# Kernel tuning notes

Measured on AMD Instinct MI355X. Metric: run time of the kernel, lower is better.

The kernel has to match this reference:

```python
import jax, jax.numpy as jnp
import numpy as np

B, S, DIM = 2, 2048, 2048
H, KVH, HD = 16, 4, 128
WIN = 512
ROPE_BASE = 10000.0
EPS = 1.1920928955078125e-07  # torch F.rms_norm default eps for fp32


def setup_inputs() -> dict:
    key = jax.random.key(0)
    ks = jax.random.split(key, 6)
    kv_dim = KVH * HD
    sc = lambda fan_in: 1.0 / np.sqrt(fan_in)
    return {
        "x": jax.random.normal(ks[0], (B, S, DIM), jnp.float32),
        "Wq": jax.random.normal(ks[1], (DIM, DIM), jnp.float32) * sc(DIM),
        "Wk": jax.random.normal(ks[2], (kv_dim, DIM), jnp.float32) * sc(DIM),
        "Wv": jax.random.normal(ks[3], (kv_dim, DIM), jnp.float32) * sc(DIM),
        "Wo": jax.random.normal(ks[4], (DIM, DIM), jnp.float32) * sc(DIM),
        "q_gain": jnp.ones((H,), jnp.float32),
    }


def _rms_norm(x):
    return x * jax.lax.rsqrt(jnp.mean(x * x, axis=-1, keepdims=True) + EPS)


def _rope_tables(seqlen, dtype):
    half = HD // 2
    inv_freq = ROPE_BASE ** (-jnp.arange(0, half, dtype=jnp.float32) / half)
    freqs = jnp.arange(seqlen, dtype=jnp.float32)[:, None] * inv_freq[None, :]  # [S, HD/2]
    return jnp.cos(freqs).astype(dtype), jnp.sin(freqs).astype(dtype)


def _apply_rotary(x, cos, sin):
    # x: [B, H, S, HD]; cos/sin: [S, HD/2]
    half = x.shape[-1] // 2
    x1, x2 = x[..., :half], x[..., half:]
    c = cos[None, None, :, :]
    s = sin[None, None, :, :]
    return jnp.concatenate([x1 * c + x2 * s, -x1 * s + x2 * c], axis=-1)


def reference(x, Wq, Wk, Wv, Wo, q_gain):
    bsz, seqlen, dim = x.shape
    q = jnp.einsum("bsd,ed->bse", x, Wq).reshape(bsz, seqlen, H, HD).transpose(0, 2, 1, 3)
    k = jnp.einsum("bsd,ed->bse", x, Wk).reshape(bsz, seqlen, KVH, HD).transpose(0, 2, 1, 3)
    v = jnp.einsum("bsd,ed->bse", x, Wv).reshape(bsz, seqlen, KVH, HD).transpose(0, 2, 1, 3)

    q = _rms_norm(q)
    k = _rms_norm(k)

    cos, sin = _rope_tables(seqlen, q.dtype)
    q = _apply_rotary(q, cos, sin)
    k = _apply_rotary(k, cos, sin)

    q = q * q_gain[None, :, None, None]

    # GQA: expand kv heads to match query heads
    rep = H // KVH
    k = jnp.repeat(k, rep, axis=1)
    v = jnp.repeat(v, rep, axis=1)

    row = jnp.arange(seqlen)[:, None]
    col = jnp.arange(seqlen)[None, :]
    mask = (col <= row) & (col >= row - WIN + 1)  # [S, S]

    scale = 1.0 / np.sqrt(HD)
    scores = jnp.einsum("bhsd,bhtd->bhst", q, k) * scale
    scores = jnp.where(mask[None, None, :, :], scores, -jnp.inf)
    attn = jax.nn.softmax(scores, axis=-1)
    y = jnp.einsum("bhst,bhtd->bhsd", attn, v)  # [B, H, S, HD]

    y = y.transpose(0, 2, 1, 3).reshape(bsz, seqlen, dim)
    return jnp.einsum("bsd,ed->bse", y, Wo)
```

## Files before the change

### kernel.cpp

```cpp
#include <hip/hip_runtime.h>

#define S_LEN 2048
#define DIM   2048
#define NH    16
#define NKV   4
#define HD    128
#define WIN   512
#define BATCH 2

typedef __bf16 bf16x8 __attribute__((ext_vector_type(8)));
typedef __bf16 bf16x4 __attribute__((ext_vector_type(4)));
typedef float  f32x4  __attribute__((ext_vector_type(4)));

union U8 { bf16x8 v; bf16x4 h[2]; };

__device__ inline void async_load16(const void* g, void* l) {
  __builtin_amdgcn_global_load_lds(
      (const __attribute__((address_space(1))) unsigned int*)g,
      (__attribute__((address_space(3))) unsigned int*)l, 16, 0, 0);
}

__global__ __launch_bounds__(256) void preprocess_kernel(
    const float* __restrict__ x,
    const float* __restrict__ Wq, const float* __restrict__ Wk,
    const float* __restrict__ Wv, const float* __restrict__ Wo,
    __bf16* __restrict__ xb, __bf16* __restrict__ wqkv, __bf16* __restrict__ wob,
    float* __restrict__ cosT, float* __restrict__ sinT) {
  const int blk = blockIdx.x, tid = threadIdx.x;
  if (blk < 8192) {
    int i = blk * 256 + tid;
    float4 v = ((const float4*)x)[i];
    bf16x4 o;
    o[0] = (__bf16)v.x; o[1] = (__bf16)v.y; o[2] = (__bf16)v.z; o[3] = (__bf16)v.w;
    ((bf16x4*)xb)[i] = o;
  } else if (blk < 18432) {
    int i = (blk - 8192) * 256 + tid;
    int orow = i >> 9, c = i & 511;
    const float* src;
    __bf16* dst;
    long soff;
    if (orow < 2048) {
      int n = orow & 127;
      int sr = (orow & ~127) + ((n >> 5) << 4) + (n & 15) + (((n >> 4) & 1) << 6);
      src = Wq; soff = (long)sr * 512 + c; dst = wqkv + (long)orow * 2048;
    } else if (orow < 2560) {
      int lr = orow - 2048, n = lr & 127;
      int sr = (lr & ~127) + ((n >> 5) << 4) + (n & 15) + (((n >> 4) & 1) << 6);
      src = Wk; soff = (long)sr * 512 + c; dst = wqkv + (long)orow * 2048;
    } else if (orow < 3072) {
      src = Wv; soff = (long)(orow - 2560) * 512 + c; dst = wqkv + (long)orow * 2048;
    } else {
      src = Wo; soff = (long)(orow - 3072) * 512 + c; dst = wob + (long)(orow - 3072) * 2048;
    }
    float4 v = ((const float4*)src)[soff];
    bf16x4 o;
    o[0] = (__bf16)v.x; o[1] = (__bf16)v.y; o[2] = (__bf16)v.z; o[3] = (__bf16)v.w;
    ((bf16x4*)dst)[c] = o;
  } else {
    int idx = (blk - 18432) * 256 + tid;
    int s = idx >> 6, d = idx & 63;
    float f = (float)s * powf(10000.f, -(float)d * (1.f / 64.f));
    float sn, cs;
    sincosf(f, &sn, &cs);
    cosT[idx] = cs;
    sinT[idx] = sn;
  }
}

__global__ __launch_bounds__(256) void gemm_bt(
    const __bf16* __restrict__ A, const __bf16* __restrict__ Bt,
    float* __restrict__ C, int M, int N, int K) {
  __shared__ __bf16 As[128 * 32];
  __shared__ __bf16 Bs[128 * 32];
  const int t = threadIdx.x;
  const int wid = t >> 6, lane = t & 63;
  const int quad = lane >> 4, l15 = lane & 15;
  const long m0 = (long)blockIdx.x * 128, n0 = (long)blockIdx.y * 128;
  const int wm = (wid >> 1) * 64, wn = (wid & 1) * 64;

  const __bf16* ga = A + (m0 + (t >> 2)) * (long)K + (t & 3) * 8;
  const __bf16* gb = Bt + (n0 + (t >> 2)) * (long)K + (t & 3) * 8;
  char* lA = (char*)As + wid * 1024;
  char* lB = (char*)Bs + wid * 1024;
  const long rstride = 64L * K;

  f32x4 zero = {0.f, 0.f, 0.f, 0.f};
  f32x4 acc[4][4];
#pragma unroll
  for (int i = 0; i < 4; ++i)
#pragma unroll
    for (int j = 0; j < 4; ++j) acc[i][j] = zero;

  for (int k0 = 0; k0 < K; k0 += 32) {
    async_load16(ga + k0, lA);
    async_load16(ga + k0 + rstride, lA + 4096);
    async_load16(gb + k0, lB);
    async_load16(gb + k0 + rstride, lB + 4096);
    __syncthreads();
    bf16x8 af[4], bfr[4];
#pragma unroll
    for (int i = 0; i < 4; ++i) {
      af[i] = *(const bf16x8*)(As + (wm + i * 16 + l15) * 32 + quad * 8);
      bfr[i] = *(const bf16x8*)(Bs + (wn + i * 16 + l15) * 32 + quad * 8);
    }
#pragma unroll
    for (int i = 0; i < 4; ++i)
#pragma unroll
      for (int j = 0; j < 4; ++j)
        acc[i][j] = __builtin_amdgcn_mfma_f32_16x16x32_bf16(af[i], bfr[j], acc[i][j], 0, 0, 0);
    __syncthreads();
  }

#pragma unroll
  for (int i = 0; i < 4; ++i)
#pragma unroll
    for (int j = 0; j < 4; ++j)
#pragma unroll
      for (int r = 0; r < 4; ++r)
        C[(m0 + wm + i * 16 + quad * 4 + r) * (long)N + n0 + wn + j * 16 + l15] = acc[i][j][r];
}

__global__ __launch_bounds__(256) void gemm_qkv(
    const __bf16* __restrict__ A, const __bf16* __restrict__ Bt,
    const float* __restrict__ gain,
    const float* __restrict__ cosT, const float* __restrict__ sinT,
    __bf16* __restrict__ Qo, __bf16* __restrict__ Ko, __bf16* __restrict__ Vt) {
  __shared__ __bf16 As[128 * 32];
  __shared__ __bf16 Bs[128 * 32];
  const int K = 2048;
  const int t = threadIdx.x;
  const int wid = t >> 6, lane = t & 63;
  const int quad = lane >> 4, l15 = lane & 15;
  const long m0 = (long)blockIdx.x * 128, n0 = (long)blockIdx.y * 128;
  const int wm = (wid >> 1) * 64, wn = (wid & 1) * 64;

  const __bf16* ga = A + (m0 + (t >> 2)) * (long)K + (t & 3) * 8;
  const __bf16* gb = Bt + (n0 + (t >> 2)) * (long)K + (t & 3) * 8;
  char* lA = (char*)As + wid * 1024;
  char* lB = (char*)Bs + wid * 1024;
  const long rstride = 64L * K;

  f32x4 zero = {0.f, 0.f, 0.f, 0.f};
  f32x4 acc[4][4];
#pragma unroll
  for (int i = 0; i < 4; ++i)
#pragma unroll
    for (int j = 0; j < 4; ++j) acc[i][j] = zero;

  for (int k0 = 0; k0 < K; k0 += 32) {
    async_load16(ga + k0, lA);
    async_load16(ga + k0 + rstride, lA + 4096);
    async_load16(gb + k0, lB);
    async_load16(gb + k0 + rstride, lB + 4096);
    __syncthreads();
    bf16x8 af[4], bfr[4];
#pragma unroll
    for (int i = 0; i < 4; ++i) {
      af[i] = *(const bf16x8*)(As + (wm + i * 16 + l15) * 32 + quad * 8);
      bfr[i] = *(const bf16x8*)(Bs + (wn + i * 16 + l15) * 32 + quad * 8);
    }
#pragma unroll
    for (int i = 0; i < 4; ++i)
#pragma unroll
      for (int j = 0; j < 4; ++j)
        acc[i][j] = __builtin_amdgcn_mfma_f32_16x16x32_bf16(af[i], bfr[j], acc[i][j], 0, 0, 0);
    __syncthreads();
  }

  const int by = blockIdx.y;
  const int srow0 = (int)(m0 & 2047);
  const int bb = (int)(m0 >> 11);

  if (by >= 20) {
    const int kvh = by - 20;
    __bf16* Vb = Vt + ((long)(bb * NKV + kvh)) * HD * S_LEN;
#pragma unroll
    for (int i = 0; i < 4; ++i)
#pragma unroll
      for (int j = 0; j < 4; ++j) {
        int d = wn + j * 16 + l15;
        int s0 = srow0 + wm + i * 16 + quad * 4;
        bf16x4 o;
#pragma unroll
        for (int r = 0; r < 4; ++r) o[r] = (__bf16)acc[i][j][r];
        *(bf16x4*)(Vb + (long)d * S_LEN + s0) = o;
      }
  } else {
    float* sums = (float*)As;
#pragma unroll
    for (int i = 0; i < 4; ++i)
#pragma unroll
      for (int r = 0; r < 4; ++r) {
        float t2 = acc[i][0][r] * acc[i][0][r] + acc[i][1][r] * acc[i][1][r] +
                   acc[i][2][r] * acc[i][2][r] + acc[i][3][r] * acc[i][3][r];
#pragma unroll
        for (int off = 1; off < 16; off <<= 1) t2 += __shfl_xor(t2, off, 64);
        if (l15 == 0) sums[(wm + i * 16 + quad * 4 + r) * 2 + (wn >> 6)] = t2;
      }
    __syncthreads();

    float g;
    __bf16* base;
    if (by < 16) {
      g = gain[by] * 0.08838834764831845f;
      base = Qo + ((long)(bb * NH + by)) * S_LEN * HD;
    } else {
      g = 1.f;
      base = Ko + ((long)(bb * NKV + (by - 16))) * S_LEN * HD;
    }
#pragma unroll
    for (int i = 0; i < 4; ++i)
#pragma unroll
      for (int r = 0; r < 4; ++r) {
        int lrow = wm + i * 16 + quad * 4 + r;
        int srow = srow0 + lrow;
        float rs = rsqrtf((sums[lrow * 2] + sums[lrow * 2 + 1]) * (1.f / 128.f) +
                          1.1920928955078125e-07f);
#pragma unroll
        for (int a = 0; a < 2; ++a) {
          int dlow = (wn >> 1) + a * 16 + l15;
          float cv = cosT[srow * 64 + dlow];
          float sv = sinT[srow * 64 + dlow];
          float x1 = acc[i][2 * a][r] * rs;
          float x2 = acc[i][2 * a + 1][r] * rs;
          base[(long)srow * HD + wn + (2 * a) * 16 + l15] = (__bf16)((x1 * cv + x2 * sv) * g);
          base[(long)srow * HD + wn + (2 * a + 1) * 16 + l15] = (__bf16)((-x1 * sv + x2 * cv) * g);
        }
      }
  }
}

__global__ __launch_bounds__(256, 4) void attn_kernel(
    const __bf16* __restrict__ Q,
    const __bf16* __restrict__ K,
    const __bf16* __restrict__ Vt,
    const float* __restrict__ gain,
    __bf16* __restrict__ Y) {
  __shared__ __bf16 Ks[64 * 128];
  __shared__ __bf16 Vs[128 * 64];
  __shared__ __bf16 Ps[4][16 * 64];

  const int t = threadIdx.x;
  const int wid = t >> 6, lane = t & 63;
  const int quad = lane >> 4, l15 = lane & 15;
  const int qt_blk = 31 - blockIdx.x;
  const int h = blockIdx.y, b = blockIdx.z;
  const int kv = h >> 2;
  const int t0 = qt_blk * 64;
  const int r0 = t0 + wid * 16;

  const __bf16* Qb = Q + ((long)(b * NH + h)) * S_LEN * HD;
  const __bf16* Kb = K + ((long)(b * NKV + kv)) * S_LEN * HD;
  const __bf16* Vb = Vt + ((long)(b * NKV + kv)) * HD * S_LEN;
  const float M = 11.3137085f * fabsf(gain[h]);

  bf16x8 qf[4];
#pragma unroll
  for (int c = 0; c < 4; ++c)
    qf[c] = *(const bf16x8*)(Qb + (long)(r0 + l15) * HD + c * 32 + quad * 8);

  f32x4 zero = {0.f, 0.f, 0.f, 0.f};
  f32x4 acc[8];
#pragma unroll
  for (int d = 0; d < 8; ++d) acc[d] = zero;
  float lac = 0.f;

  int ksrc[4], vsrc[4];
#pragma unroll
  for (int j = 0; j < 4; ++j) {
    int kr = j * 16 + (t >> 4);
    ksrc[j] = kr * HD + (((t & 15) ^ (kr & 15)) << 3);
    int vd = j * 32 + (t >> 3);
    vsrc[j] = vd * S_LEN + (((t & 7) ^ (vd & 7)) << 3);
  }

  const int kstart = (t0 >= WIN) ? (t0 - WIN) : 0;
  const int ntiles = (t0 + 64 - kstart) >> 6;

  for (int it = 0; it < ntiles; ++it) {
    const int kt = kstart + it * 64;
#pragma unroll
    for (int j = 0; j < 4; ++j) {
      async_load16(Kb + (long)kt * HD + ksrc[j], (char*)Ks + j * 4096 + t * 16);
      async_load16(Vb + kt + vsrc[j], (char*)Vs + j * 4096 + t * 16);
    }
    __syncthreads();

    if (kt <= r0 + 15 && kt + 63 >= r0 - (WIN - 1)) {
#pragma unroll
      for (int kti = 0; kti < 4; ++kti) {
        bf16x8 kf[4];
#pragma unroll
        for (int c = 0; c < 4; ++c)
          kf[c] = *(const bf16x8*)(Ks + (kti * 16 + l15) * 128 +
                                   ((((c << 2) + quad) ^ l15) << 3));
        f32x4 sc = zero;
#pragma unroll
        for (int c = 0; c < 4; ++c)
          sc = __builtin_amdgcn_mfma_f32_16x16x32_bf16(kf[c], qf[c], sc, 0, 0, 0);
        const int qg = r0 + l15;
        const int kbase = kt + kti * 16 + quad * 4;
        bf16x4 pv;
#pragma unroll
        for (int r = 0; r < 4; ++r) {
          int key = kbase + r;
          float p = (key <= qg && key >= qg - (WIN - 1)) ? __expf(sc[r] - M) : 0.f;
          lac += p;
          pv[r] = (__bf16)p;
        }
        const int cb = kti * 4 + quad;
        *(bf16x4*)(&Ps[wid][l15 * 64 + ((cb ^ l15) << 2)]) = pv;
      }
      bf16x8 pf[2];
#pragma unroll
      for (int kc = 0; kc < 2; ++kc) {
        U8 u;
        u.h[0] = *(const bf16x4*)(&Ps[wid][l15 * 64 + (((kc * 8 + quad * 2) ^ l15) << 2)]);
        u.h[1] = *(const bf16x4*)(&Ps[wid][l15 * 64 + (((kc * 8 + quad * 2 + 1) ^ l15) << 2)]);
        pf[kc] = u.v;
      }
#pragma unroll
      for (int dt = 0; dt < 8; ++dt)
#pragma unroll
        for (int kc = 0; kc < 2; ++kc) {
          bf16x8 vf = *(const bf16x8*)(Vs + (dt * 16 + l15) * 64 +
                                       ((((kc << 2) + quad) ^ (l15 & 7)) << 3));
          acc[dt] = __builtin_amdgcn_mfma_f32_16x16x32_bf16(pf[kc], vf, acc[dt], 0, 0, 0);
        }
    }
    __syncthreads();
  }

  float s = lac;
  s += __shfl_xor(s, 16, 64);
  s += __shfl_xor(s, 32, 64);
  __bf16* Yb = Y + ((long)b * S_LEN) * DIM + h * HD;
#pragma unroll
  for (int r = 0; r < 4; ++r) {
    const int row = quad * 4 + r;
    float il = 1.f / __shfl(s, row, 64);
#pragma unroll
    for (int dt = 0; dt < 8; ++dt)
      Yb[(long)(r0 + row) * DIM + dt * 16 + l15] = (__bf16)(acc[dt][r] * il);
  }
}

extern "C" void kernel_launch(void* const* d_in, const int* in_sizes, int n_in,
                              void* d_out, int out_size, void* d_ws, size_t ws_size,
                              hipStream_t stream) {
  (void)in_sizes; (void)n_in; (void)out_size; (void)ws_size;
  const float* x  = (const float*)d_in[0];
  const float* Wq = (const float*)d_in[1];
  const float* Wk = (const float*)d_in[2];
  const float* Wv = (const float*)d_in[3];
  const float* Wo = (const float*)d_in[4];
  const float* qg = (const float*)d_in[5];
  float* out = (float*)d_out;

  char* ws = (char*)d_ws;
  size_t off = 0;
  auto alloc = [&](size_t bytes) -> void* {
    void* p = ws + off;
    off += (bytes + 255) & ~(size_t)255;
    return p;
  };
  __bf16* xb   = (__bf16*)alloc(8388608ull * 2);
  __bf16* wqkv = (__bf16*)alloc(3072ull * 2048 * 2);
  __bf16* wob  = (__bf16*)alloc(2048ull * 2048 * 2);
  __bf16* qo   = (__bf16*)alloc((size_t)BATCH * NH * S_LEN * HD * 2);
  __bf16* ko   = (__bf16*)alloc((size_t)BATCH * NKV * S_LEN * HD * 2);
  __bf16* vt   = (__bf16*)alloc((size_t)BATCH * NKV * HD * S_LEN * 2);
  float*  cosT = (float*)alloc(2048ull * 64 * 4);
  float*  sinT = (float*)alloc(2048ull * 64 * 4);
  __bf16* yb   = xb;

  preprocess_kernel<<<18944, 256, 0, stream>>>(x, Wq, Wk, Wv, Wo, xb, wqkv, wob,
                                               cosT, sinT);
  gemm_qkv<<<dim3(32, 24), 256, 0, stream>>>(xb, wqkv, qg, cosT, sinT, qo, ko, vt);
  attn_kernel<<<dim3(32, 16, 2), 256, 0, stream>>>(qo, ko, vt, qg, yb);
  gemm_bt<<<dim3(32, 16), 256, 0, stream>>>(yb, wob, out, 4096, 2048, 2048);
}
```

Before: 264.1 us.

## Rewrite QKV GEMM as 256x256 tile, double-buffered, swizzled LDS pipeline

The QKV projection GEMM moves from 128x128 tiles with 256 threads and a single LDS buffer to 256x256 tiles with 512 threads (8 waves). It uses 128 KB of dynamic shared memory for double-buffered K=64 stages, XOR-swizzled LDS columns, and interleaved MFMA and prefetch phases with s_setprio. This is meant to hide global-load latency, cut LDS bank conflicts and raise data reuse per tile. The epilogue is remapped so each block covers two heads. The grid drops to 192 blocks, which may underfill the CUs and raises register pressure from 128 accumulators per thread.

Measured after the change: 274.0 us. 3.7% more time.

```diff
diff --git a/kernel.cpp b/kernel.cpp
--- a/kernel.cpp
+++ b/kernel.cpp
@@ -120,111 +120,210 @@
         C[(m0 + wm + i * 16 + quad * 4 + r) * (long)N + n0 + wn + j * 16 + l15] = acc[i][j][r];
 }
 
-__global__ __launch_bounds__(256) void gemm_qkv(
+__global__ __launch_bounds__(512, 2) void gemm_qkv(
     const __bf16* __restrict__ A, const __bf16* __restrict__ Bt,
     const float* __restrict__ gain,
     const float* __restrict__ cosT, const float* __restrict__ sinT,
     __bf16* __restrict__ Qo, __bf16* __restrict__ Ko, __bf16* __restrict__ Vt) {
-  __shared__ __bf16 As[128 * 32];
-  __shared__ __bf16 Bs[128 * 32];
-  const int K = 2048;
+  extern __shared__ char smem[];
+  constexpr int K = 2048;
+  constexpr int NT = 32;
   const int t = threadIdx.x;
   const int wid = t >> 6, lane = t & 63;
   const int quad = lane >> 4, l15 = lane & 15;
-  const long m0 = (long)blockIdx.x * 128, n0 = (long)blockIdx.y * 128;
-  const int wm = (wid >> 1) * 64, wn = (wid & 1) * 64;
-
-  const __bf16* ga = A + (m0 + (t >> 2)) * (long)K + (t & 3) * 8;
-  const __bf16* gb = Bt + (n0 + (t >> 2)) * (long)K + (t & 3) * 8;
-  char* lA = (char*)As + wid * 1024;
-  char* lB = (char*)Bs + wid * 1024;
-  const long rstride = 64L * K;
+  const int wr = wid >> 2, wc = wid & 3;
+  const long m0 = (long)blockIdx.x * 256;
+  const long n0 = (long)blockIdx.y * 256;
+
+  const int srw = (wid << 3) + (lane >> 3);
+  const int c8 = (lane & 7) ^ ((lane >> 3) & 7);
+  const __bf16* ag = A + (m0 + srw) * (long)K + c8 * 8;
+  const __bf16* bg = Bt + (n0 + srw) * (long)K + c8 * 8;
+  char* const lbase = smem + (wid << 10);
+
+  auto stage = [&](int buf, int op, int h, int j, int kt) {
+    const __bf16* g = (op ? bg : ag) + (long)((h << 7) + (j << 6)) * K + (long)kt * 64;
+    async_load16(g, lbase + buf * 65536 + op * 32768 + h * 16384 + j * 8192);
+  };
+
+  const int swz = (l15 & 7) << 4;
+  const int col0 = (quad * 16) ^ swz;
+  const int col1 = (64 + quad * 16) ^ swz;
+  const char* const aBase = smem + wr * 16384;
+  const char* const bBase = smem + 32768 + (wc >> 1) * 16384;
+  const int brow = (wc & 1) << 6;
 
   f32x4 zero = {0.f, 0.f, 0.f, 0.f};
-  f32x4 acc[4][4];
-#pragma unroll
-  for (int i = 0; i < 4; ++i)
+  f32x4 acc[8][4];
+#pragma unroll
+  for (int i = 0; i < 8; ++i)
 #pragma unroll
     for (int j = 0; j < 4; ++j) acc[i][j] = zero;
 
-  for (int k0 = 0; k0 < K; k0 += 32) {
-    async_load16(ga + k0, lA);
-    async_load16(ga + k0 + rstride, lA + 4096);
-    async_load16(gb + k0, lB);
-    async_load16(gb + k0 + rstride, lB + 4096);
-    __syncthreads();
-    bf16x8 af[4], bfr[4];
+#pragma unroll
+  for (int b = 0; b < 2; ++b)
+#pragma unroll
+    for (int op = 0; op < 2; ++op)
+#pragma unroll
+      for (int h = 0; h < 2; ++h)
+#pragma unroll
+        for (int j = 0; j < 2; ++j) stage(b, op, h, j, b);
+  asm volatile("s_waitcnt vmcnt(8)" ::: "memory");
+  __builtin_amdgcn_s_barrier();
+
+  auto group = [&](const int buf, const int tt) {
+    const char* As = aBase + buf * 65536;
+    const char* Bs = bBase + buf * 65536;
+    const bool st = (tt + 2) < NT;
+    bf16x8 afl[4][2], afh[4][2], bfl[2][2], bfh[2][2];
 #pragma unroll
     for (int i = 0; i < 4; ++i) {
-      af[i] = *(const bf16x8*)(As + (wm + i * 16 + l15) * 32 + quad * 8);
-      bfr[i] = *(const bf16x8*)(Bs + (wn + i * 16 + l15) * 32 + quad * 8);
-    }
-#pragma unroll
-    for (int i = 0; i < 4; ++i)
-#pragma unroll
-      for (int j = 0; j < 4; ++j)
-        acc[i][j] = __builtin_amdgcn_mfma_f32_16x16x32_bf16(af[i], bfr[j], acc[i][j], 0, 0, 0);
-    __syncthreads();
+      afl[i][0] = *(const bf16x8*)(As + (i * 16 + l15) * 128 + col0);
+      afl[i][1] = *(const bf16x8*)(As + (i * 16 + l15) * 128 + col1);
+    }
+#pragma unroll
+    for (int j = 0; j < 2; ++j) {
+      bfl[j][0] = *(const bf16x8*)(Bs + (brow + j * 16 + l15) * 128 + col0);
+      bfl[j][1] = *(const bf16x8*)(Bs + (brow + j * 16 + l15) * 128 + col1);
+    }
+    __builtin_amdgcn_s_barrier();
+    asm volatile("s_waitcnt lgkmcnt(0)" ::: "memory");
+    __builtin_amdgcn_s_setprio(1);
+#pragma unroll
+    for (int kk = 0; kk < 2; ++kk)
+#pragma unroll
+      for (int i = 0; i < 4; ++i)
+#pragma unroll
+        for (int j = 0; j < 2; ++j)
+          acc[i][j] = __builtin_amdgcn_mfma_f32_16x16x32_bf16(afl[i][kk], bfl[j][kk],
+                                                              acc[i][j], 0, 0, 0);
+    __builtin_amdgcn_s_setprio(0);
+    __builtin_amdgcn_s_barrier();
+#pragma unroll
+    for (int i = 0; i < 4; ++i) {
+      afh[i][0] = *(const bf16x8*)(As + ((i + 4) * 16 + l15) * 128 + col0);
+      afh[i][1] = *(const bf16x8*)(As + ((i + 4) * 16 + l15) * 128 + col1);
+    }
+    __builtin_amdgcn_s_barrier();
+    asm volatile("s_waitcnt lgkmcnt(0)" ::: "memory");
+    __builtin_amdgcn_s_setprio(1);
+#pragma unroll
+    for (int kk = 0; kk < 2; ++kk)
+#pragma unroll
+      for (int i = 0; i < 4; ++i)
+#pragma unroll
+        for (int j = 0; j < 2; ++j)
+          acc[i + 4][j] = __builtin_amdgcn_mfma_f32_16x16x32_bf16(afh[i][kk], bfl[j][kk],
+                                                                  acc[i + 4][j], 0, 0, 0);
+    __builtin_amdgcn_s_setprio(0);
+    __builtin_amdgcn_s_barrier();
+#pragma unroll
+    for (int j = 0; j < 2; ++j) {
+      bfh[j][0] = *(const bf16x8*)(Bs + (brow + (j + 2) * 16 + l15) * 128 + col0);
+      bfh[j][1] = *(const bf16x8*)(Bs + (brow + (j + 2) * 16 + l15) * 128 + col1);
+    }
+    if (st) { stage(buf, 0, 0, 0, tt + 2); stage(buf, 0, 0, 1, tt + 2); }
+    __builtin_amdgcn_s_barrier();
+    asm volatile("s_waitcnt lgkmcnt(0)" ::: "memory");
+    __builtin_amdgcn_s_setprio(1);
+#pragma unroll
+    for (int kk = 0; kk < 2; ++kk)
+#pragma unroll
+      for (int i = 0; i < 4; ++i)
+#pragma unroll
+        for (int j = 0; j < 2; ++j)
+          acc[i + 4][j + 2] = __builtin_amdgcn_mfma_f32_16x16x32_bf16(afh[i][kk], bfh[j][kk],
+                                                                      acc[i + 4][j + 2], 0, 0, 0);
+    __builtin_amdgcn_s_setprio(0);
+    __builtin_amdgcn_s_barrier();
+    if (st) {
+      stage(buf, 0, 1, 0, tt + 2); stage(buf, 0, 1, 1, tt + 2);
+      stage(buf, 1, 0, 0, tt + 2); stage(buf, 1, 0, 1, tt + 2);
+      stage(buf, 1, 1, 0, tt + 2); stage(buf, 1, 1, 1, tt + 2);
+      asm volatile("s_waitcnt vmcnt(8)" ::: "memory");
+    } else {
+      asm volatile("s_waitcnt vmcnt(0)" ::: "memory");
+    }
+    __builtin_amdgcn_s_barrier();
+    __builtin_amdgcn_s_setprio(1);
+#pragma unroll
+    for (int kk = 0; kk < 2; ++kk)
+#pragma unroll
+      for (int i = 0; i < 4; ++i)
+#pragma unroll
+        for (int j = 0; j < 2; ++j)
+          acc[i][j + 2] = __builtin_amdgcn_mfma_f32_16x16x32_bf16(afl[i][kk], bfh[j][kk],
+                                                                  acc[i][j + 2], 0, 0, 0);
+    __builtin_amdgcn_s_setprio(0);
+    __builtin_amdgcn_s_barrier();
+  };
+
+  for (int tt = 0; tt < NT; tt += 2) {
+    group(0, tt);
+    group(1, tt + 1);
   }
 
   const int by = blockIdx.y;
   const int srow0 = (int)(m0 & 2047);
   const int bb = (int)(m0 >> 11);
 
-  if (by >= 20) {
-    const int kvh = by - 20;
+  if (by >= 10) {
+    const int kvh = (by - 10) * 2 + (wc >> 1);
     __bf16* Vb = Vt + ((long)(bb * NKV + kvh)) * HD * S_LEN;
 #pragma unroll
-    for (int i = 0; i < 4; ++i)
+    for (int i = 0; i < 8; ++i)
 #pragma unroll
       for (int j = 0; j < 4; ++j) {
-        int d = wn + j * 16 + l15;
-        int s0 = srow0 + wm + i * 16 + quad * 4;
+        const int d = brow + j * 16 + l15;
+        const int s0 = srow0 + wr * 128 + i * 16 + quad * 4;
         bf16x4 o;
 #pragma unroll
         for (int r = 0; r < 4; ++r) o[r] = (__bf16)acc[i][j][r];
         *(bf16x4*)(Vb + (long)d * S_LEN + s0) = o;
       }
   } else {
-    float* sums = (float*)As;
-#pragma unroll
-    for (int i = 0; i < 4; ++i)
+    float* sums = (float*)smem;
+#pragma unroll
+    for (int i = 0; i < 8; ++i)
 #pragma unroll
       for (int r = 0; r < 4; ++r) {
         float t2 = acc[i][0][r] * acc[i][0][r] + acc[i][1][r] * acc[i][1][r] +
                    acc[i][2][r] * acc[i][2][r] + acc[i][3][r] * acc[i][3][r];
 #pragma unroll
         for (int off = 1; off < 16; off <<= 1) t2 += __shfl_xor(t2, off, 64);
-        if (l15 == 0) sums[(wm + i * 16 + quad * 4 + r) * 2 + (wn >> 6)] = t2;
+        if (l15 == 0) sums[(wr * 128 + i * 16 + quad * 4 + r) * 4 + wc] = t2;
       }
     __syncthreads();
 
     float g;
     __bf16* base;
-    if (by < 16) {
-      g = gain[by] * 0.08838834764831845f;
-      base = Qo + ((long)(bb * NH + by)) * S_LEN * HD;
+    if (by < 8) {
+      const int h = by * 2 + (wc >> 1);
+      g = gain[h] * 0.08838834764831845f;
+      base = Qo + ((long)(bb * NH + h)) * S_LEN * HD;
     } else {
+      const int h = (by - 8) * 2 + (wc >> 1);
       g = 1.f;
-      base = Ko + ((long)(bb * NKV + (by - 16))) * S_LEN * HD;
-    }
-#pragma unroll
-    for (int i = 0; i < 4; ++i)
+      base = Ko + ((long)(bb * NKV + h)) * S_LEN * HD;
+    }
+#pragma unroll
+    for (int i = 0; i < 8; ++i)
 #pragma unroll
       for (int r = 0; r < 4; ++r) {
-        int lrow = wm + i * 16 + quad * 4 + r;
-        int srow = srow0 + lrow;
-        float rs = rsqrtf((sums[lrow * 2] + sums[lrow * 2 + 1]) * (1.f / 128.f) +
-                          1.1920928955078125e-07f);
+        const int lrow = wr * 128 + i * 16 + quad * 4 + r;
+        const int srow = srow0 + lrow;
+        const float rs = rsqrtf((sums[lrow * 4 + (wc & 2)] + sums[lrow * 4 + (wc & 2) + 1]) *
+                                    (1.f / 128.f) +
+                                1.1920928955078125e-07f);
 #pragma unroll
         for (int a = 0; a < 2; ++a) {
-          int dlow = (wn >> 1) + a * 16 + l15;
-          float cv = cosT[srow * 64 + dlow];
-          float sv = sinT[srow * 64 + dlow];
-          float x1 = acc[i][2 * a][r] * rs;
-          float x2 = acc[i][2 * a + 1][r] * rs;
-          base[(long)srow * HD + wn + (2 * a) * 16 + l15] = (__bf16)((x1 * cv + x2 * sv) * g);
-          base[(long)srow * HD + wn + (2 * a + 1) * 16 + l15] = (__bf16)((-x1 * sv + x2 * cv) * g);
+          const int dlow = ((wc & 1) << 5) + a * 16 + l15;
+          const float cv = cosT[srow * 64 + dlow];
+          const float sv = sinT[srow * 64 + dlow];
+          const float x1 = acc[i][2 * a][r] * rs;
+          const float x2 = acc[i][2 * a + 1][r] * rs;
+          base[(long)srow * HD + brow + (2 * a) * 16 + l15] = (__bf16)((x1 * cv + x2 * sv) * g);
+          base[(long)srow * HD + brow + (2 * a + 1) * 16 + l15] = (__bf16)((-x1 * sv + x2 * cv) * g);
         }
       }
   }
@@ -374,9 +473,12 @@
   float*  sinT = (float*)alloc(2048ull * 64 * 4);
   __bf16* yb   = xb;
 
+  (void)hipFuncSetAttribute((const void*)gemm_qkv,
+                            hipFuncAttributeMaxDynamicSharedMemorySize, 131072);
+
   preprocess_kernel<<<18944, 256, 0, stream>>>(x, Wq, Wk, Wv, Wo, xb, wqkv, wob,
                                                cosT, sinT);
-  gemm_qkv<<<dim3(32, 24), 256, 0, stream>>>(xb, wqkv, qg, cosT, sinT, qo, ko, vt);
+  gemm_qkv<<<dim3(16, 12), 512, 131072, stream>>>(xb, wqkv, qg, cosT, sinT, qo, ko, vt);
   attn_kernel<<<dim3(32, 16, 2), 256, 0, stream>>>(qo, ko, vt, qg, yb);
   gemm_bt<<<dim3(32, 16), 256, 0, stream>>>(yb, wob, out, 4096, 2048, 2048);
 }
```
